# Optimization experiments

Measured on AMD Instinct MI355X. Metric: run time of the kernel, lower is better.

Reference implementation:

```python
import jax, jax.numpy as jnp
import numpy as np

STRIDE = (4, 4)
MASK = (17, 17)
G_MEAN = 85.384
G_STD = 53.798
LEV = 5  # len(bins)
EPS = 1e-8
_BINS = np.array([0.0, 0.5, G_MEAN - G_STD, G_MEAN, G_MEAN + G_STD], dtype=np.float32)
_DISTS = [1, 2, 4]
_THETAS = [0.0, np.pi / 4, np.pi / 2, 3 * np.pi / 4]
# skimage greycomatrix offsets: (row, col) = (round(sin(t)*d), round(cos(t)*d)), dist-major
OFFSETS = [(int(round(np.sin(t) * d)), int(round(np.cos(t) * d))) for d in _DISTS for t in _THETAS]


def setup_inputs():
    key = jax.random.key(0)
    x = jax.random.uniform(key, (8, 1, 512, 512), dtype=jnp.float32) * 255.0
    return {"inputs": x}


def _sliding_windows(x):
    B, C, H, W = x.shape
    nx = (H - MASK[0]) // STRIDE[0] + 1
    ny = (W - MASK[1]) // STRIDE[1] + 1
    rows = (jnp.arange(nx) * STRIDE[0])[:, None] + jnp.arange(MASK[0])  # (nx, Mx)
    cols = (jnp.arange(ny) * STRIDE[1])[:, None] + jnp.arange(MASK[1])  # (ny, My)
    w = x[:, :, rows]              # (B, C, nx, Mx, W)
    w = w[:, :, :, :, cols]        # (B, C, nx, Mx, ny, My)
    return jnp.transpose(w, (0, 1, 2, 4, 3, 5))  # (B, C, nx, ny, Mx, My)


def _statistics(w):
    m = w.mean(axis=(-2, -1))
    s = w.std(axis=(-2, -1))
    mx = w.max(axis=(-2, -1))
    mn = w.min(axis=(-2, -1))
    # Faithful to original: mean is rescaled in-place BEFORE being used in max/min stats
    m = m / G_MEAN
    s = s / G_STD
    mx = (mx - m) / G_STD
    mn = (m - mn) / G_STD
    return jnp.concatenate([m, s, mx, mn], axis=1)  # (B, 4*C, nx, ny)


def _glcm(qf, dr, dc):
    # qf: (Wn, Mx, My) int32 -> normalized symmetric GLCM (Wn, LEV, LEV)
    Mx, My = qf.shape[-2:]
    if dc >= 0:
        a = qf[:, :Mx - dr, :My - dc]
        b = qf[:, dr:, dc:]
    else:
        a = qf[:, :Mx - dr, -dc:]
        b = qf[:, dr:, :My + dc]
    Wn = qf.shape[0]
    code = (a * LEV + b).reshape(Wn, -1)
    flat = (jnp.arange(Wn, dtype=jnp.int32)[:, None] * (LEV * LEV) + code).reshape(-1)
    cnt = jax.ops.segment_sum(jnp.ones(flat.shape, jnp.float32), flat, num_segments=Wn * LEV * LEV)
    G = cnt.reshape(Wn, LEV, LEV)
    G = G + jnp.swapaxes(G, -1, -2)  # symmetric=True
    return G / jnp.sum(G, axis=(-2, -1), keepdims=True)  # normed=True


def _hist_glcm_features(q):
    # q: (B, C, nx, ny, Mx, My) int32 -> (B, 64, nx, ny) (C must be 1)
    B, C, nx, ny, Mx, My = q.shape
    qf = q.reshape(-1, Mx, My)
    Wn = qf.shape[0]
    G = jnp.stack([_glcm(qf, dr, dc) for dr, dc in OFFSETS], axis=1)  # (Wn, 12, L, L)

    I = jnp.arange(LEV, dtype=jnp.float32)
    d2 = (I[:, None] - I[None, :]) ** 2
    contrast = jnp.einsum('wkij,ij->wk', G, d2)
    homogeneity = jnp.einsum('wkij,ij->wk', G, 1.0 / (1.0 + d2))
    energy = jnp.sqrt(jnp.sum(G * G, axis=(-2, -1)))
    Pi = G.sum(axis=-1)   # (Wn, 12, L)
    Pj = G.sum(axis=-2)
    mu_i = jnp.sum(I * Pi, axis=-1)
    mu_j = jnp.sum(I * Pj, axis=-1)
    di = I[None, None, :] - mu_i[..., None]
    dj = I[None, None, :] - mu_j[..., None]
    std_i = jnp.sqrt(jnp.sum(Pi * di * di, axis=-1))
    std_j = jnp.sqrt(jnp.sum(Pj * dj * dj, axis=-1))
    cov = jnp.einsum('wkij,wki,wkj->wk', G, di, dj)
    denom = std_i * std_j
    correlation = jnp.where(denom < 1e-15, 1.0, cov / jnp.maximum(denom, 1e-30))
    entropy = -jnp.sum(G * jnp.log2(G + EPS), axis=(-2, -1))  # (Wn, 12)

    qv = qf.reshape(Wn, -1)
    cnts = jnp.stack([jnp.sum(qv == k, axis=-1) for k in range(1, LEV)], axis=-1).astype(jnp.float32)
    tot = cnts.sum(axis=-1, keepdims=True)
    hist = jnp.where(tot > 0, cnts / jnp.maximum(tot, 1.0), 0.0)  # (Wn, LEV-1)

    feat = jnp.concatenate([hist, contrast, homogeneity, energy, correlation, entropy], axis=-1)
    feat = feat.reshape(B, C, nx, ny, -1)
    return jnp.transpose(feat, (0, 4, 2, 3, 1))[..., 0]  # (B, 64, nx, ny)


def reference(inputs):
    w = _sliding_windows(inputs)                                   # (B,C,nx,ny,17,17)
    stat = _statistics(w)                                          # (B,4,nx,ny)
    q = (jnp.digitize(w, jnp.asarray(_BINS)) - 1).astype(jnp.int32)
    hg = _hist_glcm_features(q)                                    # (B,64,nx,ny)
    feats = jnp.concatenate([stat, hg], axis=1)                    # (B,68,nx,ny)
    return jnp.mean(feats, axis=(-2, -1))                          # (B,68)
```

## Files before the change

### kernel.cpp

```cpp
#include <hip/hip_runtime.h>


#define G_MEAN_F 85.384f
#define G_STD_F  53.798f
#define MASK_WS_BYTES (8u * 512u * 36u * 8u)

__device__ constexpr int LO15[15] = {0,0,0,0,0,1,1,1,1,2,2,2,3,3,4};
__device__ constexpr int HI15[15] = {0,1,2,3,4,1,2,3,4,2,3,4,3,4,4};

__device__ __forceinline__ float wred(float v) {
#pragma unroll
  for (int m = 32; m; m >>= 1) v += __shfl_xor(v, m, 64);
  return v;
}

__device__ __forceinline__ void load_sl(const unsigned* sl, int idx, unsigned m[5]) {
  const uint4 q = *(const uint4*)(sl + idx * 4);
  m[1] = q.x; m[2] = q.y; m[3] = q.z; m[4] = q.w;
  m[0] = 0x1FFFFu & ~(m[1] | m[2] | m[3] | m[4]);
}

template<int DC>
__device__ __forceinline__ void updoff(unsigned* cnt, const unsigned a[5], const unsigned b[5]) {
  unsigned as[5], bs[5];
#pragma unroll
  for (int v = 0; v < 5; ++v) {
    as[v] = (DC < 0) ? (a[v] >> (-DC)) : a[v];
    bs[v] = (DC > 0) ? (b[v] >> DC) : b[v];
  }
#pragma unroll
  for (int u = 0; u < 15; ++u) {
    const int i = LO15[u], j = HI15[u];
    unsigned t = as[i] & bs[j];
    if (i != j) t |= as[j] & bs[i];
    cnt[u] += __popc(t);
  }
}

__device__ __forceinline__ void feat5(const unsigned* cnt, float Np,
                                      float& con, float& hom, float& ene,
                                      float& corr, float& ent) {
  const float invN = 1.0f / Np;
  const float inv2N = 0.5f / Np;
  con = 0.0f; hom = 0.0f; ent = 0.0f;
  float eac = 0.0f;
  float P[5] = {0, 0, 0, 0, 0};
#pragma unroll
  for (int u = 0; u < 15; ++u) {
    const int lo = LO15[u], hi = HI15[u];
    const float m = (float)cnt[u];
    const float d2 = (float)((hi - lo) * (hi - lo));
    con += m * d2;
    hom += m * (1.0f / (1.0f + d2));
    if (lo == hi) {
      eac += m * m;
      P[lo] += 2.0f * m;
      float g = m * invN;
      ent -= g * __log2f(g + 1e-8f);
    } else {
      eac += 0.5f * m * m;
      P[lo] += m; P[hi] += m;
      float g = m * inv2N;
      ent -= 2.0f * g * __log2f(g + 1e-8f);
    }
  }
  con *= invN;
  hom *= invN;
  ene = sqrtf(eac) * invN;
  float mu = 0.0f;
#pragma unroll
  for (int i = 0; i < 5; ++i) { P[i] *= inv2N; mu += (float)i * P[i]; }
  float s2 = 0.0f;
#pragma unroll
  for (int i = 0; i < 5; ++i) { float d = (float)i - mu; s2 = fmaf(P[i] * d, d, s2); }
  float denom = s2;
  float cov = 0.0f;
#pragma unroll
  for (int u = 0; u < 15; ++u)
    cov += ((float)cnt[u] * invN) * ((float)LO15[u] - mu) * ((float)HI15[u] - mu);
  corr = (denom < 1e-15f) ? 1.0f : cov / fmaxf(denom, 1e-30f);
}

__device__ __forceinline__ void emit2(const unsigned c1[15], const unsigned c2[15], float Np,
                                      bool v1, bool v2, float* pt0, int k0, int k1) {
  float con1, hom1, ene1, cor1, ent1, con2, hom2, ene2, cor2, ent2;
  feat5(c1, Np, con1, hom1, ene1, cor1, ent1);
  feat5(c2, Np, con2, hom2, ene2, cor2, ent2);
  if (!v1) { con1 = 0; hom1 = 0; ene1 = 0; cor1 = 0; ent1 = 0; }
  if (!v2) { con2 = 0; hom2 = 0; ene2 = 0; cor2 = 0; ent2 = 0; }
  float con = wred(con1 + con2), hom = wred(hom1 + hom2), ene = wred(ene1 + ene2);
  float cor = wred(cor1 + cor2), ent = wred(ent1 + ent2);
  if ((threadIdx.x & 63) == 0) {
    const float s = 1.0f / 15376.0f;
    pt0[(8 + k0) * 128] = con * s;
    pt0[(20 + k0) * 128] = hom * s;
    pt0[(32 + k0) * 128] = ene * s;
    pt0[(44 + k0) * 128] = cor * s;
    pt0[(56 + k0) * 128] = ent * s;
    if (k1 >= 0) {
      pt0[(8 + k1) * 128] = con * s;
      pt0[(20 + k1) * 128] = hom * s;
      pt0[(32 + k1) * 128] = ene * s;
      pt0[(44 + k1) * 128] = cor * s;
      pt0[(56 + k1) * 128] = ent * s;
    }
  }
}

template<int DR, int DC>
__device__ void glcm2(const unsigned* sl, int s, int ly, bool v1, bool v2,
                      float Np, float* pt0, int k0, int k1) {
  unsigned A[15], S[15], B[15];
#pragma unroll
  for (int u = 0; u < 15; ++u) { A[u] = 0; S[u] = 0; B[u] = 0; }
  unsigned buf[DR > 0 ? DR : 1][5];
  if constexpr (DR > 0) {
#pragma unroll
    for (int i = 0; i < DR; ++i) load_sl(sl, (s + i) * 8 + ly, buf[i]);
  }
  unsigned nxt[5];
  load_sl(sl, (s + DR) * 8 + ly, nxt);

#define SEGRUN(CNT, RB, RE)                                              \
  _Pragma("unroll 1")                                                    \
  for (int R = (RB); R < (RE); ++R) {                                    \
    unsigned cur[5];                                                     \
    _Pragma("unroll")                                                    \
    for (int v = 0; v < 5; ++v) cur[v] = nxt[v];                         \
    load_sl(sl, (s + DR + R + 1) * 8 + ly, nxt);  \
    if constexpr (DR > 0) {                                              \
      updoff<DC>(CNT, buf[0], cur);                                      \
      _Pragma("unroll")                                                  \
      for (int i = 0; i < DR - 1; ++i)                                   \
        _Pragma("unroll")                                                \
        for (int v = 0; v < 5; ++v) buf[i][v] = buf[i + 1][v];           \
      _Pragma("unroll")                                                  \
      for (int v = 0; v < 5; ++v) buf[DR > 0 ? DR - 1 : 0][v] = cur[v];  \
    } else {                                                             \
      updoff<DC>(CNT, cur, cur);                                         \
    }                                                                    \
  }

  SEGRUN(A, 0, 4)
  SEGRUN(S, 4, 17 - DR)
  SEGRUN(B, 17 - DR, 21 - DR)
#undef SEGRUN

#pragma unroll
  for (int u = 0; u < 15; ++u) { A[u] += S[u]; B[u] += S[u]; }
  emit2(A, B, Np, v1, v2, pt0, k0, k1);
}

__global__ __launch_bounds__(64)
void mask_build_kernel(const float* __restrict__ x, unsigned long long* __restrict__ mg) {
  const int lane = threadIdx.x;
  const int r = blockIdx.x;
  const int b = blockIdx.y;
  const float* xr = x + ((size_t)b * 512 + r) * 512;
  unsigned long long* mr = mg + ((size_t)b * 512 + r) * 36;

  const float T1 = 0.5f;
  const float T2 = (float)(85.384 - 53.798);
  const float T3 = 85.384f;
  const float T4 = (float)(85.384 + 53.798);

#pragma unroll 1
  for (int seg = 0; seg < 8; ++seg) {
    float xv = xr[seg * 64 + lane];
    int q = (int)(xv >= T1) + (int)(xv >= T2) + (int)(xv >= T3) + (int)(xv >= T4);
    unsigned long long b1 = __ballot(q == 1);
    unsigned long long b2 = __ballot(q == 2);
    unsigned long long b3 = __ballot(q == 3);
    unsigned long long b4 = __ballot(q == 4);
    if (lane < 4) {
      unsigned long long bv = (lane == 0) ? b1 : (lane == 1) ? b2 : (lane == 2) ? b3 : b4;
      mr[seg * 4 + lane] = bv;
    }
  }
  if (lane < 4) mr[32 + lane] = 0;
}

__global__ __launch_bounds__(256)
void glcm_feat_kernel(const float* __restrict__ x,
                      const unsigned long long* __restrict__ mg,
                      float* __restrict__ part) {
  __shared__ __align__(16) unsigned sl[79 * 8 * 4];

  const int tid = threadIdx.x;
  const int lane = tid & 63;
  const int ty = blockIdx.x;
  const int txg = blockIdx.y;
  const int tx = txg / 3;
  const int g = txg - tx * 3;
  const int role = g * 4 + (tid >> 6);
  const int b = blockIdx.z;
  const int px0 = tx * 64;
  const int py0 = ty * 32;
  const float* xb = x + (size_t)b * 512 * 512;

  const int s0 = py0 >> 6;
  const int sh = py0 & 63;
  const unsigned long long* mgb = mg + (size_t)b * 512 * 36 + s0 * 4;
#pragma unroll 1
  for (int t = tid; t < 79 * 8; t += 256) {
    const int row = t >> 3, ly = t & 7;
    unsigned sv[4] = {0, 0, 0, 0};
    if (row < 77) {
      int gr = px0 + row; if (gr > 511) gr = 511;
      const unsigned long long* p = mgb + (size_t)gr * 36;
#pragma unroll
      for (int lev = 0; lev < 4; ++lev) {
        unsigned long long cmb = p[lev];
        if (sh) cmb = (cmb >> 32) | (p[4 + lev] << 32);
        sv[lev] = (unsigned)(cmb >> (4 * ly)) & 0x1FFFFu;
      }
    }
    *(uint4*)(sl + t * 4) = make_uint4(sv[0], sv[1], sv[2], sv[3]);
  }
  __syncthreads();

  const int lxp = lane >> 3, ly = lane & 7;
  const int wx1 = tx * 16 + 2 * lxp;
  const int wy = ty * 8 + ly;
  const bool vy = (wy < 124);
  const bool v1 = (wx1 < 124) && vy;
  const bool v2 = (wx1 + 1 < 124) && vy;
  const int s = 8 * lxp;
  const int tile = tx * 16 + ty;
  float* pt0 = part + (size_t)b * 68 * 128 + tile;

  if (role == 0) {
    int sp = px0 + s; if (sp > 488) sp = 488;
    int c0 = py0 + 4 * ly; if (c0 > 492) c0 = 492;
    const float* fw = xb + (size_t)sp * 512 + c0;
    float sA = 0, qA = 0, sS = 0, qS = 0, sB = 0, qB = 0;
    float mxA = -1e30f, mnA = 1e30f, mxS = -1e30f, mnS = 1e30f, mxB = -1e30f, mnB = 1e30f;
#pragma unroll 1
    for (int r = 0; r < 21; ++r) {
      const float* p = fw + r * 512;
      const float4* p4 = (const float4*)p;
      float rs = 0, rq = 0, rmx = -1e30f, rmn = 1e30f;
#pragma unroll
      for (int w = 0; w < 4; ++w) {
        float4 f = p4[w];
        rs += f.x; rq = fmaf(f.x, f.x, rq); rmx = fmaxf(rmx, f.x); rmn = fminf(rmn, f.x);
        rs += f.y; rq = fmaf(f.y, f.y, rq); rmx = fmaxf(rmx, f.y); rmn = fminf(rmn, f.y);
        rs += f.z; rq = fmaf(f.z, f.z, rq); rmx = fmaxf(rmx, f.z); rmn = fminf(rmn, f.z);
        rs += f.w; rq = fmaf(f.w, f.w, rq); rmx = fmaxf(rmx, f.w); rmn = fminf(rmn, f.w);
      }
      float t = p[16];
      rs += t; rq = fmaf(t, t, rq); rmx = fmaxf(rmx, t); rmn = fminf(rmn, t);
      if (r < 4)       { sA += rs; qA += rq; mxA = fmaxf(mxA, rmx); mnA = fminf(mnA, rmn); }
      else if (r < 17) { sS += rs; qS += rq; mxS = fmaxf(mxS, rmx); mnS = fminf(mnS, rmn); }
      else             { sB += rs; qB += rq; mxB = fmaxf(mxB, rmx); mnB = fminf(mnB, rmn); }
    }
    float ch[4][2];
#pragma unroll
    for (int w = 0; w < 2; ++w) {
      float sum = w ? (sS + sB) : (sA + sS);
      float ssq = w ? (qS + qB) : (qA + qS);
      float mx = w ? fmaxf(mxS, mxB) : fmaxf(mxA, mxS);
      float mn = w ? fminf(mnS, mnB) : fminf(mnA, mnS);
      float mean = sum * (1.0f / 289.0f);
      float var = fmaxf(ssq * (1.0f / 289.0f) - mean * mean, 0.0f);
      float fm = mean / G_MEAN_F;
      ch[0][w] = fm;
      ch[1][w] = sqrtf(var) / G_STD_F;
      ch[2][w] = (mx - fm) / G_STD_F;
      ch[3][w] = (fm - mn) / G_STD_F;
    }
#pragma unroll
    for (int c = 0; c < 4; ++c) {
      float f = (v1 ? ch[c][0] : 0.0f) + (v2 ? ch[c][1] : 0.0f);
      f = wred(f);
      if (lane == 0) pt0[c * 128] = f * (1.0f / 15376.0f);
    }
  } else if (role == 1) {
    unsigned hA[4] = {0,0,0,0}, hS[4] = {0,0,0,0}, hB[4] = {0,0,0,0};
#pragma unroll 1
    for (int R = 0; R < 21; ++R) {
      const uint4 q = *(const uint4*)(sl + ((s + R) * 8 + ly) * 4);
      unsigned* h = (R < 4) ? hA : (R < 17) ? hS : hB;
      h[0] += __popc(q.x); h[1] += __popc(q.y); h[2] += __popc(q.z); h[3] += __popc(q.w);
    }
    float ch[4][2];
#pragma unroll
    for (int w = 0; w < 2; ++w) {
      unsigned t1 = w ? (hS[0] + hB[0]) : (hA[0] + hS[0]);
      unsigned t2 = w ? (hS[1] + hB[1]) : (hA[1] + hS[1]);
      unsigned t3 = w ? (hS[2] + hB[2]) : (hA[2] + hS[2]);
      unsigned t4 = w ? (hS[3] + hB[3]) : (hA[3] + hS[3]);
      unsigned tot = t1 + t2 + t3 + t4;
      float ti = (tot > 0) ? 1.0f / (float)tot : 0.0f;
      ch[0][w] = (float)t1 * ti;
      ch[1][w] = (float)t2 * ti;
      ch[2][w] = (float)t3 * ti;
      ch[3][w] = (float)t4 * ti;
    }
#pragma unroll
    for (int c = 0; c < 4; ++c) {
      float f = (v1 ? ch[c][0] : 0.0f) + (v2 ? ch[c][1] : 0.0f);
      f = wred(f);
      if (lane == 0) pt0[(4 + c) * 128] = f * (1.0f / 15376.0f);
    }
  } else if (role == 2) {
    glcm2<0, 1>(sl, s, ly, v1, v2, 272.0f, pt0, 0, -1);
  } else if (role == 3) {
    glcm2<1, 0>(sl, s, ly, v1, v2, 272.0f, pt0, 2, -1);
  } else if (role == 4) {
    glcm2<0, 2>(sl, s, ly, v1, v2, 255.0f, pt0, 4, -1);
  } else if (role == 5) {
    glcm2<1, 1>(sl, s, ly, v1, v2, 256.0f, pt0, 1, 5);
  } else if (role == 6) {
    glcm2<0, 4>(sl, s, ly, v1, v2, 221.0f, pt0, 8, -1);
  } else if (role == 7) {
    glcm2<1, -1>(sl, s, ly, v1, v2, 256.0f, pt0, 3, 7);
  } else if (role == 8) {
    glcm2<2, 0>(sl, s, ly, v1, v2, 255.0f, pt0, 6, -1);
  } else if (role == 9) {
    glcm2<3, 3>(sl, s, ly, v1, v2, 196.0f, pt0, 9, -1);
  } else if (role == 10) {
    glcm2<4, 0>(sl, s, ly, v1, v2, 221.0f, pt0, 10, -1);
  } else {
    glcm2<3, -3>(sl, s, ly, v1, v2, 196.0f, pt0, 11, -1);
  }
}

__global__ __launch_bounds__(64)
void reduce_kernel(const float* __restrict__ part, float* __restrict__ out) {
  const int ch = blockIdx.x;
  const int b = blockIdx.y;
  const int lane = threadIdx.x;
  const float2* p = (const float2*)(part + ((size_t)b * 68 + ch) * 128);
  float2 f = p[lane];
  float v = f.x + f.y;
  v = wred(v);
  if (lane == 0) out[b * 68 + ch] = v;
}

extern "C" void kernel_launch(void* const* d_in, const int* in_sizes, int n_in,
                              void* d_out, int out_size, void* d_ws, size_t ws_size,
                              hipStream_t stream)
{
  const float* x = (const float*)d_in[0];
  float* out = (float*)d_out;
  unsigned long long* mg = (unsigned long long*)d_ws;
  float* part = (float*)((char*)d_ws + MASK_WS_BYTES);

  mask_build_kernel<<<dim3(512, 8), dim3(64), 0, stream>>>(x, mg);
  glcm_feat_kernel<<<dim3(16, 24, 8), dim3(256), 0, stream>>>(x, mg, part);
  reduce_kernel<<<dim3(68, 8), dim3(64), 0, stream>>>(part, out);
}
```

Before: 113.1 us.

## Pack GLCM counters into 10-bit fields and reload distant rows from LDS

The 15 co-occurrence counters per segment are packed three per 32-bit register in 10-bit fields, cutting the accumulator set from 45 registers to 15. For row offsets greater than one, the rolling buffer of previous rows is replaced by a second LDS load per iteration. The launch bounds now request higher occupancy (256 threads, 8 blocks). This trades extra LDS traffic and shift/mask work for lower register pressure. The 10-bit fields hold at most 1023, which the per-window counts (at most 17x17 pairs per segment) stay below.

```diff
diff --git a/kernel.cpp b/kernel.cpp
--- a/kernel.cpp
+++ b/kernel.cpp
@@ -21,7 +21,7 @@
 }
 
 template<int DC>
-__device__ __forceinline__ void updoff(unsigned* cnt, const unsigned a[5], const unsigned b[5]) {
+__device__ __forceinline__ void updoff_pk(unsigned* pk, const unsigned a[5], const unsigned b[5]) {
   unsigned as[5], bs[5];
 #pragma unroll
   for (int v = 0; v < 5; ++v) {
@@ -33,7 +33,7 @@
     const int i = LO15[u], j = HI15[u];
     unsigned t = as[i] & bs[j];
     if (i != j) t |= as[j] & bs[i];
-    cnt[u] += __popc(t);
+    pk[u / 3] += (unsigned)__popc(t) << ((u % 3) * 10);
   }
 }
 
@@ -110,16 +110,16 @@
 template<int DR, int DC>
 __device__ void glcm2(const unsigned* sl, int s, int ly, bool v1, bool v2,
                       float Np, float* pt0, int k0, int k1) {
-  unsigned A[15], S[15], B[15];
-#pragma unroll
-  for (int u = 0; u < 15; ++u) { A[u] = 0; S[u] = 0; B[u] = 0; }
-  unsigned buf[DR > 0 ? DR : 1][5];
-  if constexpr (DR > 0) {
-#pragma unroll
-    for (int i = 0; i < DR; ++i) load_sl(sl, (s + i) * 8 + ly, buf[i]);
-  }
-  unsigned nxt[5];
-  load_sl(sl, (s + DR) * 8 + ly, nxt);
+  unsigned pA[5] = {0,0,0,0,0}, pS[5] = {0,0,0,0,0}, pB[5] = {0,0,0,0,0};
+
+  if constexpr (DR <= 1) {
+    unsigned buf[DR > 0 ? DR : 1][5];
+    if constexpr (DR > 0) {
+#pragma unroll
+      for (int i = 0; i < DR; ++i) load_sl(sl, (s + i) * 8 + ly, buf[i]);
+    }
+    unsigned nxt[5];
+    load_sl(sl, (s + DR) * 8 + ly, nxt);
 
 #define SEGRUN(CNT, RB, RE)                                              \
   _Pragma("unroll 1")                                                    \
@@ -129,25 +129,50 @@
     for (int v = 0; v < 5; ++v) cur[v] = nxt[v];                         \
     load_sl(sl, (s + DR + R + 1) * 8 + ly, nxt);  \
     if constexpr (DR > 0) {                                              \
-      updoff<DC>(CNT, buf[0], cur);                                      \
+      updoff_pk<DC>(CNT, buf[0], cur);                                   \
       _Pragma("unroll")                                                  \
-      for (int i = 0; i < DR - 1; ++i)                                   \
-        _Pragma("unroll")                                                \
-        for (int v = 0; v < 5; ++v) buf[i][v] = buf[i + 1][v];           \
-      _Pragma("unroll")                                                  \
-      for (int v = 0; v < 5; ++v) buf[DR > 0 ? DR - 1 : 0][v] = cur[v];  \
+      for (int v = 0; v < 5; ++v) buf[0][v] = cur[v];                    \
     } else {                                                             \
-      updoff<DC>(CNT, cur, cur);                                         \
+      updoff_pk<DC>(CNT, cur, cur);                                      \
     }                                                                    \
   }
 
-  SEGRUN(A, 0, 4)
-  SEGRUN(S, 4, 17 - DR)
-  SEGRUN(B, 17 - DR, 21 - DR)
+    SEGRUN(pA, 0, 4)
+    SEGRUN(pS, 4, 17 - DR)
+    SEGRUN(pB, 17 - DR, 21 - DR)
 #undef SEGRUN
-
-#pragma unroll
-  for (int u = 0; u < 15; ++u) { A[u] += S[u]; B[u] += S[u]; }
+  } else {
+    unsigned nxtA[5], nxtB[5];
+    load_sl(sl, s * 8 + ly, nxtA);
+    load_sl(sl, (s + DR) * 8 + ly, nxtB);
+
+#define SEGRUN2(CNT, RB, RE)                                             \
+  _Pragma("unroll 1")                                                    \
+  for (int R = (RB); R < (RE); ++R) {                                    \
+    unsigned curA[5], curB[5];                                           \
+    _Pragma("unroll")                                                    \
+    for (int v = 0; v < 5; ++v) { curA[v] = nxtA[v]; curB[v] = nxtB[v]; }\
+    load_sl(sl, (s + R + 1) * 8 + ly, nxtA);      \
+    load_sl(sl, (s + R + 1 + DR) * 8 + ly, nxtB); \
+    updoff_pk<DC>(CNT, curA, curB);                                      \
+  }
+
+    SEGRUN2(pA, 0, 4)
+    SEGRUN2(pS, 4, 17 - DR)
+    SEGRUN2(pB, 17 - DR, 21 - DR)
+#undef SEGRUN2
+  }
+
+  unsigned A[15], B[15];
+#pragma unroll
+  for (int u = 0; u < 15; ++u) {
+    const int sh = (u % 3) * 10;
+    const unsigned a_ = (pA[u / 3] >> sh) & 0x3FFu;
+    const unsigned s_ = (pS[u / 3] >> sh) & 0x3FFu;
+    const unsigned b_ = (pB[u / 3] >> sh) & 0x3FFu;
+    A[u] = a_ + s_;
+    B[u] = b_ + s_;
+  }
   emit2(A, B, Np, v1, v2, pt0, k0, k1);
 }
 
@@ -180,7 +205,7 @@
   if (lane < 4) mr[32 + lane] = 0;
 }
 
-__global__ __launch_bounds__(256)
+__global__ __launch_bounds__(256, 8)
 void glcm_feat_kernel(const float* __restrict__ x,
                       const unsigned long long* __restrict__ mg,
                       float* __restrict__ part) {
```

Result: no change. 112.9 us (-0.2%).
